# Kernel tuning notes

Hardware: AMD Instinct MI355X
Metric: run time of the kernel (lower is better)

Reference implementation:

```python
import jax, jax.numpy as jnp
import numpy as np

B, T, C = 4, 2048, 1024
H, Dh = 16, 64
EPS = 1e-5

def _layernorm(x, g, b):
    mu = jnp.mean(x, axis=-1, keepdims=True)
    var = jnp.mean(jnp.square(x - mu), axis=-1, keepdims=True)
    return (x - mu) * jax.lax.rsqrt(var + EPS) * g + b

def setup_inputs() -> dict:
    key = jax.random.key(0)
    ks = jax.random.split(key, 12)
    s = lambda fan_in: 1.0 / np.sqrt(fan_in)
    return {
        "x":  jax.random.normal(ks[0], (B, T, C), dtype=jnp.float32),
        "Wq": jax.random.uniform(ks[1], (C, H * Dh), jnp.float32, -s(C), s(C)),
        "Wk": jax.random.uniform(ks[2], (C, H * Dh), jnp.float32, -s(C), s(C)),
        "Wv": jax.random.uniform(ks[3], (C, H * Dh), jnp.float32, -s(C), s(C)),
        "Wo": jax.random.uniform(ks[4], (H * Dh, C), jnp.float32, -s(H * Dh), s(H * Dh)),
        "bo": jnp.zeros((C,), jnp.float32),
        "W1": jax.random.uniform(ks[5], (C, 4 * C), jnp.float32, -s(C), s(C)),
        "b1": jnp.zeros((4 * C,), jnp.float32),
        "W2": jax.random.uniform(ks[6], (4 * C, C), jnp.float32, -s(4 * C), s(4 * C)),
        "b2": jnp.zeros((C,), jnp.float32),
        "g1": jnp.ones((C,), jnp.float32),
        "be1": jnp.zeros((C,), jnp.float32),
        "g2": jnp.ones((C,), jnp.float32),
        "be2": jnp.zeros((C,), jnp.float32),
    }

def reference(x, Wq, Wk, Wv, Wo, bo, W1, b1, W2, b2, g1, be1, g2, be2):
    # --- pre-LN attention ---
    h = _layernorm(x, g1, be1)                                   # [B,T,C]
    q = (h @ Wq).reshape(B, T, H, Dh)                            # per-head projections fused
    k = (h @ Wk).reshape(B, T, H, Dh)
    v = (h @ Wv).reshape(B, T, H, Dh)
    scores = jnp.einsum('bqhd,bkhd->bhqk', q, k) * (Dh ** -0.5)  # [B,H,T,T]
    causal = jnp.tril(jnp.ones((T, T), dtype=bool))
    scores = jnp.where(causal, scores, -jnp.inf)
    wei = jax.nn.softmax(scores, axis=-1)                        # dropout p=0 (eval)
    attn = jnp.einsum('bhqk,bkhd->bqhd', wei, v).reshape(B, T, H * Dh)
    x = x + attn @ Wo + bo
    # --- pre-LN MLP ---
    h2 = _layernorm(x, g2, be2)
    x = x + jax.nn.relu(h2 @ W1 + b1) @ W2 + b2
    return x
```

## Files before the change

### kernel.cpp

```cpp
#include <hip/hip_runtime.h>
#include <hip/hip_bf16.h>

typedef __hip_bfloat16 bf16;
typedef __attribute__((ext_vector_type(8))) short short8;
typedef __attribute__((ext_vector_type(4))) float f32x4;

__device__ __forceinline__ float s2f(short s) {
    unsigned u = ((unsigned)(unsigned short)s) << 16;
    return __builtin_bit_cast(float, u);
}
__device__ __forceinline__ short f2s(float f) {
    bf16 h = __float2bfloat16(f);
    return __builtin_bit_cast(short, h);
}
__device__ __forceinline__ void gload_lds16(const void* g, void* l) {
    __builtin_amdgcn_global_load_lds(
        (const __attribute__((address_space(1))) unsigned int*)g,
        (__attribute__((address_space(3))) unsigned int*)l, 16, 0, 0);
}

__global__ __launch_bounds__(256) void tconv_kernel(const float* __restrict__ src,
                                                    short* __restrict__ dst,
                                                    int R, int C) {
    __shared__ short tile[64][65];
    const int r0 = blockIdx.y * 64, c0 = blockIdx.x * 64;
    const int t = threadIdx.x;
    const int lr = t >> 2, lc = (t & 3) * 16;
    const float* sp = src + (size_t)(r0 + lr) * C + c0 + lc;
#pragma unroll
    for (int q = 0; q < 4; q++) {
        f32x4 v = *(const f32x4*)(const void*)(sp + q * 4);
#pragma unroll
        for (int j = 0; j < 4; j++) tile[lr][lc + q * 4 + j] = f2s(v[j]);
    }
    __syncthreads();
    short8 o0, o1;
#pragma unroll
    for (int j = 0; j < 8; j++) { o0[j] = tile[lc + j][lr]; o1[j] = tile[lc + 8 + j][lr]; }
    short* dp = dst + (size_t)(c0 + lr) * R + r0 + lc;
    *(short8*)(void*)dp = o0;
    *(short8*)(void*)(dp + 8) = o1;
}

__global__ __launch_bounds__(256) void ln_kernel(const void* __restrict__ x, int x_f32,
                                                 const float* __restrict__ g,
                                                 const float* __restrict__ beta,
                                                 bf16* __restrict__ out) {
    const int row = blockIdx.x;
    const int t = threadIdx.x;
    float v[4];
    if (x_f32) {
        const float* xr = (const float*)x + (size_t)row * 1024 + t * 4;
        f32x4 xv = *(const f32x4*)(const void*)xr;
#pragma unroll
        for (int j = 0; j < 4; j++) v[j] = xv[j];
    } else {
        const short* xr = (const short*)x + (size_t)row * 1024 + t * 4;
#pragma unroll
        for (int j = 0; j < 4; j++) v[j] = s2f(xr[j]);
    }
    float s = 0.f, ss = 0.f;
#pragma unroll
    for (int j = 0; j < 4; j++) { s += v[j]; ss += v[j] * v[j]; }
#pragma unroll
    for (int off = 32; off >= 1; off >>= 1) {
        s += __shfl_xor(s, off);
        ss += __shfl_xor(ss, off);
    }
    __shared__ float red[8];
    const int wave = t >> 6;
    if ((t & 63) == 0) { red[wave] = s; red[4 + wave] = ss; }
    __syncthreads();
    s = red[0] + red[1] + red[2] + red[3];
    ss = red[4] + red[5] + red[6] + red[7];
    const float mu = s * (1.0f / 1024.0f);
    const float var = ss * (1.0f / 1024.0f) - mu * mu;
    const float rstd = rsqrtf(var + 1e-5f);
    bf16* orow = out + (size_t)row * 1024;
#pragma unroll
    for (int j = 0; j < 4; j++) {
        const int c = t * 4 + j;
        float hv = (v[j] - mu) * rstd * g[c] + beta[c];
        orow[c] = __float2bfloat16(hv);
    }
}

__global__ __launch_bounds__(256) void gemm128(const bf16* __restrict__ A,
                                               const bf16* __restrict__ Bt,
                                               const float* __restrict__ bias,
                                               const float* resid,
                                               void* Cp, int c_f32,
                                               int m_base, int N, int K,
                                               int relu_flag) {
    __shared__ short As[128 * 32];
    __shared__ short Bs[128 * 32];

    const int t = threadIdx.x;
    const int m0 = blockIdx.y * 128;
    const int n0 = blockIdx.x * 128;
    const int w = t >> 6;
    const int lane = t & 63;
    const int wm = (w >> 1) * 64;
    const int wn = (w & 1) * 64;

    const int ar = t >> 2, ak = (t & 3) * 8;
    const bf16* aA0 = A + (size_t)(m0 + ar) * K + ak;
    const bf16* aA1 = A + (size_t)(m0 + 64 + ar) * K + ak;
    const bf16* aB0 = Bt + (size_t)(n0 + ar) * K + ak;
    const bf16* aB1 = Bt + (size_t)(n0 + 64 + ar) * K + ak;
    short* ldsA0 = &As[w * 512];
    short* ldsA1 = &As[2048 + w * 512];
    short* ldsB0 = &Bs[w * 512];
    short* ldsB1 = &Bs[2048 + w * 512];

    const int l = lane & 15;
    const int lk = (lane >> 4) * 8;

    f32x4 acc[4][4] = {};

    for (int k0 = 0; k0 < K; k0 += 32) {
        __syncthreads();
        gload_lds16(aA0 + k0, ldsA0);
        gload_lds16(aA1 + k0, ldsA1);
        gload_lds16(aB0 + k0, ldsB0);
        gload_lds16(aB1 + k0, ldsB1);
        __syncthreads();

        short8 af[4], bfv[4];
#pragma unroll
        for (int mi = 0; mi < 4; mi++)
            af[mi] = *(const short8*)&As[(wm + mi * 16 + l) * 32 + lk];
#pragma unroll
        for (int ni = 0; ni < 4; ni++)
            bfv[ni] = *(const short8*)&Bs[(wn + ni * 16 + l) * 32 + lk];
#pragma unroll
        for (int mi = 0; mi < 4; mi++)
#pragma unroll
            for (int ni = 0; ni < 4; ni++)
                acc[mi][ni] = __builtin_amdgcn_mfma_f32_16x16x32_bf16(
                    af[mi], bfv[ni], acc[mi][ni], 0, 0, 0);
    }

    const int lrow4 = (lane >> 4) * 4;
#pragma unroll
    for (int mi = 0; mi < 4; mi++)
#pragma unroll
        for (int r = 0; r < 4; r++) {
            const int grow = m_base + m0 + wm + mi * 16 + lrow4 + r;
#pragma unroll
            for (int ni = 0; ni < 4; ni++) {
                const int gcol = n0 + wn + ni * 16 + l;
                float val = acc[mi][ni][r];
                if (bias) val += bias[gcol];
                if (relu_flag) val = fmaxf(val, 0.f);
                const size_t ci = (size_t)grow * N + gcol;
                if (resid) val += resid[ci];
                if (c_f32) ((float*)Cp)[ci] = val;
                else        ((short*)Cp)[ci] = f2s(val);
            }
        }
}

__global__ __launch_bounds__(256) void gemm64(const bf16* __restrict__ A,
                                              const bf16* __restrict__ Bt,
                                              const float* __restrict__ bias,
                                              const float* resid,
                                              void* Cp, int c_f32,
                                              int m_base, int N, int K,
                                              int relu_flag) {
    __shared__ short As[64 * 64];
    __shared__ short Bs[64 * 64];

    const int t = threadIdx.x;
    const int m0 = blockIdx.x * 64;
    const int n0 = blockIdx.y * 64;
    const int w = t >> 6;
    const int lane = t & 63;
    const int wm = (w >> 1) * 32;
    const int wn = (w & 1) * 32;

    const int sr = t >> 2, sk = (t & 3) * 8;
    const bf16* aA = A + (size_t)(m0 + sr) * K + sk;
    const bf16* aB = Bt + (size_t)(n0 + sr) * K + sk;
    short* ldsA0 = &As[w * 512];
    short* ldsA1 = &As[2048 + w * 512];
    short* ldsB0 = &Bs[w * 512];
    short* ldsB1 = &Bs[2048 + w * 512];

    const int l = lane & 15;
    const int lk = (lane >> 4) * 8;

    f32x4 acc[2][2] = {};

    for (int k0 = 0; k0 < K; k0 += 64) {
        __syncthreads();
        gload_lds16(aA + k0, ldsA0);
        gload_lds16(aA + k0 + 32, ldsA1);
        gload_lds16(aB + k0, ldsB0);
        gload_lds16(aB + k0 + 32, ldsB1);
        __syncthreads();
#pragma unroll
        for (int ks = 0; ks < 2; ks++) {
            short8 a0 = *(const short8*)&As[ks * 2048 + (wm + l) * 32 + lk];
            short8 a1 = *(const short8*)&As[ks * 2048 + (wm + 16 + l) * 32 + lk];
            short8 b0 = *(const short8*)&Bs[ks * 2048 + (wn + l) * 32 + lk];
            short8 b1 = *(const short8*)&Bs[ks * 2048 + (wn + 16 + l) * 32 + lk];
            acc[0][0] = __builtin_amdgcn_mfma_f32_16x16x32_bf16(a0, b0, acc[0][0], 0, 0, 0);
            acc[0][1] = __builtin_amdgcn_mfma_f32_16x16x32_bf16(a0, b1, acc[0][1], 0, 0, 0);
            acc[1][0] = __builtin_amdgcn_mfma_f32_16x16x32_bf16(a1, b0, acc[1][0], 0, 0, 0);
            acc[1][1] = __builtin_amdgcn_mfma_f32_16x16x32_bf16(a1, b1, acc[1][1], 0, 0, 0);
        }
    }

    const int lrow4 = (lane >> 4) * 4;
#pragma unroll
    for (int mi = 0; mi < 2; mi++)
#pragma unroll
        for (int r = 0; r < 4; r++) {
            const int grow = m_base + m0 + wm + mi * 16 + lrow4 + r;
#pragma unroll
            for (int ni = 0; ni < 2; ni++) {
                const int gcol = n0 + wn + ni * 16 + l;
                float val = acc[mi][ni][r];
                if (bias) val += bias[gcol];
                if (relu_flag) val = fmaxf(val, 0.f);
                const size_t ci = (size_t)grow * N + gcol;
                if (resid) val += resid[ci];
                if (c_f32) ((float*)Cp)[ci] = val;
                else        ((short*)Cp)[ci] = f2s(val);
            }
        }
}

__global__ __launch_bounds__(256) void attn_kernel(const bf16* __restrict__ qkv,
                                                   bf16* __restrict__ o) {
    __shared__ short Ks[64][72];
    __shared__ short Vt[64][72];
    __shared__ short Pl[4][32][72];

    const int bh = blockIdx.x;
    const int b = bh >> 4, h = bh & 15;
    const int qt = 15 - blockIdx.y;
    const int q0 = qt * 128;
    const size_t rbase = (size_t)b * 2048;
    const int hcol = h * 64;

    const int t = threadIdx.x;
    const int w = t >> 6;
    const int lane = t & 63;
    const int l = lane & 15;
    const int g = lane >> 4;
    const int sp = t >> 3;
    const int sb = (t & 7) * 8;

    const int qw0 = q0 + 32 * w;
    short8 qf[2][2];
#pragma unroll
    for (int mi = 0; mi < 2; mi++)
#pragma unroll
        for (int ks = 0; ks < 2; ks++) {
            const short* qp = (const short*)qkv +
                (rbase + qw0 + mi * 16 + l) * 3072 + hcol + ks * 32 + g * 8;
            short8 tv = *(const short8*)(const void*)qp;
            short8 sv;
#pragma unroll
            for (int e = 0; e < 8; e++) sv[e] = f2s(s2f(tv[e]) * 0.125f);
            qf[mi][ks] = sv;
        }

    f32x4 o_acc[2][4] = {};
    f32x4 l_acc[2] = {};
    short8 onesf;
    {
        const short ov = (l == 0) ? (short)0x3F80 : (short)0;
#pragma unroll
        for (int e = 0; e < 8; e++) onesf[e] = ov;
    }
    const f32x4 s_init = {-12.f, -12.f, -12.f, -12.f};

    const int kt_max = (q0 + 127) >> 6;
    for (int kt = 0; kt <= kt_max; kt++) {
        const int k0 = kt * 64;
        const short* kg = (const short*)qkv + (rbase + k0 + 2 * sp) * 3072 + 1024 + hcol + sb;
        const short* vg = (const short*)qkv + (rbase + k0 + 2 * sp) * 3072 + 2048 + hcol + sb;
        short8 kv0 = *(const short8*)(const void*)kg;
        short8 kv1 = *(const short8*)(const void*)(kg + 3072);
        short8 vv0 = *(const short8*)(const void*)vg;
        short8 vv1 = *(const short8*)(const void*)(vg + 3072);
        __syncthreads();
        *(short8*)&Ks[2 * sp][sb] = kv0;
        *(short8*)&Ks[2 * sp + 1][sb] = kv1;
        {
            const int key = 2 * sp;
            const int cbk = key >> 3;
            const int kin = key & 7;
#pragma unroll
            for (int j = 0; j < 8; j++) {
                const int d = sb + j;
                const int col = ((cbk ^ (d >> 3)) << 3) + kin;
                int pk = (int)(unsigned short)vv0[j] | ((int)(unsigned short)vv1[j] << 16);
                *(int*)(void*)&Vt[d][col] = pk;
            }
        }
        __syncthreads();

        if (k0 <= qw0 + 31) {
            const bool needMask = (k0 + 63 > qw0);
            f32x4 s_acc[2][4];
#pragma unroll
            for (int mi = 0; mi < 2; mi++)
#pragma unroll
                for (int ni = 0; ni < 4; ni++) s_acc[mi][ni] = s_init;
#pragma unroll
            for (int ks = 0; ks < 2; ks++) {
                short8 kf[4];
#pragma unroll
                for (int ni = 0; ni < 4; ni++)
                    kf[ni] = *(const short8*)&Ks[ni * 16 + l][ks * 32 + g * 8];
#pragma unroll
                for (int mi = 0; mi < 2; mi++)
#pragma unroll
                    for (int ni = 0; ni < 4; ni++)
                        s_acc[mi][ni] = __builtin_amdgcn_mfma_f32_16x16x32_bf16(
                            qf[mi][ks], kf[ni], s_acc[mi][ni], 0, 0, 0);
            }
#pragma unroll
            for (int mi = 0; mi < 2; mi++)
#pragma unroll
                for (int r = 0; r < 4; r++) {
                    const int qg = qw0 + mi * 16 + 4 * g + r;
#pragma unroll
                    for (int ni = 0; ni < 4; ni++) {
                        float s = s_acc[mi][ni][r];
                        if (needMask && (k0 + ni * 16 + l > qg)) s = -1e30f;
                        Pl[w][mi * 16 + 4 * g + r][ni * 16 + l] = f2s(__expf(s));
                    }
                }
#pragma unroll
            for (int ks = 0; ks < 2; ks++) {
                short8 pf[2], vf[4];
#pragma unroll
                for (int mi = 0; mi < 2; mi++)
                    pf[mi] = *(const short8*)&Pl[w][mi * 16 + l][ks * 32 + g * 8];
#pragma unroll
                for (int nd = 0; nd < 4; nd++) {
                    const int d = nd * 16 + l;
                    const int cb = ks * 4 + g;
                    vf[nd] = *(const short8*)&Vt[d][((cb ^ (d >> 3)) << 3)];
                }
#pragma unroll
                for (int mi = 0; mi < 2; mi++) {
                    l_acc[mi] = __builtin_amdgcn_mfma_f32_16x16x32_bf16(
                        pf[mi], onesf, l_acc[mi], 0, 0, 0);
#pragma unroll
                    for (int nd = 0; nd < 4; nd++)
                        o_acc[mi][nd] = __builtin_amdgcn_mfma_f32_16x16x32_bf16(
                            pf[mi], vf[nd], o_acc[mi][nd], 0, 0, 0);
                }
            }
        }
    }

#pragma unroll
    for (int mi = 0; mi < 2; mi++)
#pragma unroll
        for (int r = 0; r < 4; r++) {
            float lsum = __shfl(l_acc[mi][r], lane & 48);
            const float inv = 1.0f / lsum;
            const int qg = qw0 + mi * 16 + 4 * g + r;
            short* op = (short*)(void*)(o + (rbase + qg) * 1024 + hcol);
#pragma unroll
            for (int nd = 0; nd < 4; nd++)
                op[nd * 16 + l] = f2s(o_acc[mi][nd][r] * inv);
        }
}

extern "C" void kernel_launch(void* const* d_in, const int* in_sizes, int n_in,
                              void* d_out, int out_size, void* d_ws, size_t ws_size,
                              hipStream_t stream) {
    const float* x   = (const float*)d_in[0];
    const float* Wq  = (const float*)d_in[1];
    const float* Wk  = (const float*)d_in[2];
    const float* Wv  = (const float*)d_in[3];
    const float* Wo  = (const float*)d_in[4];
    const float* bo  = (const float*)d_in[5];
    const float* W1  = (const float*)d_in[6];
    const float* b1  = (const float*)d_in[7];
    const float* W2  = (const float*)d_in[8];
    const float* b2  = (const float*)d_in[9];
    const float* g1  = (const float*)d_in[10];
    const float* be1 = (const float*)d_in[11];
    const float* g2  = (const float*)d_in[12];
    const float* be2 = (const float*)d_in[13];

    char* ws = (char*)d_ws;
    const size_t MB = (size_t)1024 * 1024;
    bf16*  s0  = (bf16*)(ws);
    bf16*  qkv = (bf16*)(ws + 16 * MB);
    short* WoT = (short*)(ws + 16 * MB);
    short* W1T = (short*)(ws);
    short* W2T = (short*)(ws + 8 * MB);
    bf16*  h2  = (bf16*)(ws + 16 * MB);
    bf16*  m1  = (bf16*)(ws + 32 * MB);
    short* WT  = (short*)d_out;
    float* x1  = (float*)d_out;

    const int M = 8192, C = 1024, F = 4096, MH = 4096;

    tconv_kernel<<<dim3(16, 16), 256, 0, stream>>>(Wq, WT,                   C, C);
    tconv_kernel<<<dim3(16, 16), 256, 0, stream>>>(Wk, WT + 1024 * 1024,     C, C);
    tconv_kernel<<<dim3(16, 16), 256, 0, stream>>>(Wv, WT + 2 * 1024 * 1024, C, C);

    ln_kernel<<<M, 256, 0, stream>>>(x, 1, g1, be1, s0);

    gemm128<<<dim3(3072 / 128, M / 128), 256, 0, stream>>>(
        s0, (const bf16*)WT, nullptr, nullptr, qkv, 0, 0, 3072, C, 0);

    attn_kernel<<<dim3(64, 16), 256, 0, stream>>>(qkv, s0);

    tconv_kernel<<<dim3(16, 16), 256, 0, stream>>>(Wo, WoT, C, C);
    gemm64<<<dim3(M / 64, C / 64), 256, 0, stream>>>(
        s0, (const bf16*)WoT, bo, x, x1, 1, 0, C, C, 0);

    tconv_kernel<<<dim3(64, 16), 256, 0, stream>>>(W1, W1T, C, F);
    tconv_kernel<<<dim3(16, 64), 256, 0, stream>>>(W2, W2T, F, C);

    ln_kernel<<<M, 256, 0, stream>>>(x1, 1, g2, be2, h2);

    for (int half = 0; half < 2; half++) {
        const bf16* Ah = h2 + (size_t)half * MH * C;
        gemm128<<<dim3(F / 128, MH / 128), 256, 0, stream>>>(
            Ah, (const bf16*)W1T, b1, nullptr, m1, 0, 0, F, C, 1);
        gemm64<<<dim3(MH / 64, C / 64), 256, 0, stream>>>(
            m1, (const bf16*)W2T, b2, x1, d_out, 1, half * MH, C, F, 0);
    }
}
```

Baseline: 627.0 us.

## Use wave-per-row layernorm, async swizzled K loads, and gemm64 for all GEMMs

Layernorm now gives each wavefront one row with vectorized loads and stores, which drops the LDS reduction and block barrier. The attention kernel loads K tiles straight into LDS with global_load_lds using an XOR-swizzled layout instead of staging them through registers. gemm128 is removed, so the QKV and W1 GEMMs now use the 64x64 tiled gemm64. Smaller tiles cut reuse per block but launch more blocks, which may help occupancy or may raise memory traffic.

```diff
diff --git a/kernel.cpp b/kernel.cpp
--- a/kernel.cpp
+++ b/kernel.cpp
@@ -3,6 +3,7 @@
 
 typedef __hip_bfloat16 bf16;
 typedef __attribute__((ext_vector_type(8))) short short8;
+typedef __attribute__((ext_vector_type(4))) short s16x4;
 typedef __attribute__((ext_vector_type(4))) float f32x4;
 
 __device__ __forceinline__ float s2f(short s) {
@@ -42,123 +43,46 @@
     *(short8*)(void*)(dp + 8) = o1;
 }
 
-__global__ __launch_bounds__(256) void ln_kernel(const void* __restrict__ x, int x_f32,
+__global__ __launch_bounds__(256) void ln_kernel(const float* __restrict__ x,
                                                  const float* __restrict__ g,
                                                  const float* __restrict__ beta,
                                                  bf16* __restrict__ out) {
-    const int row = blockIdx.x;
     const int t = threadIdx.x;
-    float v[4];
-    if (x_f32) {
-        const float* xr = (const float*)x + (size_t)row * 1024 + t * 4;
-        f32x4 xv = *(const f32x4*)(const void*)xr;
-#pragma unroll
-        for (int j = 0; j < 4; j++) v[j] = xv[j];
-    } else {
-        const short* xr = (const short*)x + (size_t)row * 1024 + t * 4;
-#pragma unroll
-        for (int j = 0; j < 4; j++) v[j] = s2f(xr[j]);
-    }
+    const int w = t >> 6, lane = t & 63;
+    const int row = blockIdx.x * 4 + w;
+    const float* xr = x + (size_t)row * 1024;
+    float v[16];
     float s = 0.f, ss = 0.f;
 #pragma unroll
-    for (int j = 0; j < 4; j++) { s += v[j]; ss += v[j] * v[j]; }
+    for (int p = 0; p < 4; p++) {
+        f32x4 xv = *(const f32x4*)(const void*)(xr + p * 256 + lane * 4);
+#pragma unroll
+        for (int j = 0; j < 4; j++) {
+            v[p * 4 + j] = xv[j];
+            s += xv[j];
+            ss += xv[j] * xv[j];
+        }
+    }
 #pragma unroll
     for (int off = 32; off >= 1; off >>= 1) {
         s += __shfl_xor(s, off);
         ss += __shfl_xor(ss, off);
     }
-    __shared__ float red[8];
-    const int wave = t >> 6;
-    if ((t & 63) == 0) { red[wave] = s; red[4 + wave] = ss; }
-    __syncthreads();
-    s = red[0] + red[1] + red[2] + red[3];
-    ss = red[4] + red[5] + red[6] + red[7];
     const float mu = s * (1.0f / 1024.0f);
     const float var = ss * (1.0f / 1024.0f) - mu * mu;
     const float rstd = rsqrtf(var + 1e-5f);
-    bf16* orow = out + (size_t)row * 1024;
-#pragma unroll
-    for (int j = 0; j < 4; j++) {
-        const int c = t * 4 + j;
-        float hv = (v[j] - mu) * rstd * g[c] + beta[c];
-        orow[c] = __float2bfloat16(hv);
-    }
-}
-
-__global__ __launch_bounds__(256) void gemm128(const bf16* __restrict__ A,
-                                               const bf16* __restrict__ Bt,
-                                               const float* __restrict__ bias,
-                                               const float* resid,
-                                               void* Cp, int c_f32,
-                                               int m_base, int N, int K,
-                                               int relu_flag) {
-    __shared__ short As[128 * 32];
-    __shared__ short Bs[128 * 32];
-
-    const int t = threadIdx.x;
-    const int m0 = blockIdx.y * 128;
-    const int n0 = blockIdx.x * 128;
-    const int w = t >> 6;
-    const int lane = t & 63;
-    const int wm = (w >> 1) * 64;
-    const int wn = (w & 1) * 64;
-
-    const int ar = t >> 2, ak = (t & 3) * 8;
-    const bf16* aA0 = A + (size_t)(m0 + ar) * K + ak;
-    const bf16* aA1 = A + (size_t)(m0 + 64 + ar) * K + ak;
-    const bf16* aB0 = Bt + (size_t)(n0 + ar) * K + ak;
-    const bf16* aB1 = Bt + (size_t)(n0 + 64 + ar) * K + ak;
-    short* ldsA0 = &As[w * 512];
-    short* ldsA1 = &As[2048 + w * 512];
-    short* ldsB0 = &Bs[w * 512];
-    short* ldsB1 = &Bs[2048 + w * 512];
-
-    const int l = lane & 15;
-    const int lk = (lane >> 4) * 8;
-
-    f32x4 acc[4][4] = {};
-
-    for (int k0 = 0; k0 < K; k0 += 32) {
-        __syncthreads();
-        gload_lds16(aA0 + k0, ldsA0);
-        gload_lds16(aA1 + k0, ldsA1);
-        gload_lds16(aB0 + k0, ldsB0);
-        gload_lds16(aB1 + k0, ldsB1);
-        __syncthreads();
-
-        short8 af[4], bfv[4];
-#pragma unroll
-        for (int mi = 0; mi < 4; mi++)
-            af[mi] = *(const short8*)&As[(wm + mi * 16 + l) * 32 + lk];
-#pragma unroll
-        for (int ni = 0; ni < 4; ni++)
-            bfv[ni] = *(const short8*)&Bs[(wn + ni * 16 + l) * 32 + lk];
-#pragma unroll
-        for (int mi = 0; mi < 4; mi++)
-#pragma unroll
-            for (int ni = 0; ni < 4; ni++)
-                acc[mi][ni] = __builtin_amdgcn_mfma_f32_16x16x32_bf16(
-                    af[mi], bfv[ni], acc[mi][ni], 0, 0, 0);
-    }
-
-    const int lrow4 = (lane >> 4) * 4;
-#pragma unroll
-    for (int mi = 0; mi < 4; mi++)
-#pragma unroll
-        for (int r = 0; r < 4; r++) {
-            const int grow = m_base + m0 + wm + mi * 16 + lrow4 + r;
-#pragma unroll
-            for (int ni = 0; ni < 4; ni++) {
-                const int gcol = n0 + wn + ni * 16 + l;
-                float val = acc[mi][ni][r];
-                if (bias) val += bias[gcol];
-                if (relu_flag) val = fmaxf(val, 0.f);
-                const size_t ci = (size_t)grow * N + gcol;
-                if (resid) val += resid[ci];
-                if (c_f32) ((float*)Cp)[ci] = val;
-                else        ((short*)Cp)[ci] = f2s(val);
-            }
-        }
+    short* orow = (short*)(void*)(out + (size_t)row * 1024);
+#pragma unroll
+    for (int p = 0; p < 4; p++) {
+        const int c = p * 256 + lane * 4;
+        f32x4 gv = *(const f32x4*)(const void*)(g + c);
+        f32x4 bv = *(const f32x4*)(const void*)(beta + c);
+        s16x4 o;
+#pragma unroll
+        for (int j = 0; j < 4; j++)
+            o[j] = f2s((v[p * 4 + j] - mu) * rstd * gv[j] + bv[j]);
+        *(s16x4*)(void*)(orow + c) = o;
+    }
 }
 
 __global__ __launch_bounds__(256) void gemm64(const bf16* __restrict__ A,
@@ -234,7 +158,7 @@
 
 __global__ __launch_bounds__(256) void attn_kernel(const bf16* __restrict__ qkv,
                                                    bf16* __restrict__ o) {
-    __shared__ short Ks[64][72];
+    __shared__ short KsF[64 * 64];
     __shared__ short Vt[64][72];
     __shared__ short Pl[4][32][72];
 
@@ -268,6 +192,13 @@
             qf[mi][ks] = sv;
         }
 
+    const int key_a = w * 16 + (lane >> 3);
+    const int kd = (lane & 7) ^ ((lane >> 3) & 7);
+    const short* kgA = (const short*)qkv + (rbase + key_a) * 3072 + 1024 + hcol + kd * 8;
+    const short* kgB = kgA + 8 * 3072;
+    short* kdstA = &KsF[w * 1024];
+    short* kdstB = &KsF[w * 1024 + 512];
+
     f32x4 o_acc[2][4] = {};
     f32x4 l_acc[2] = {};
     short8 onesf;
@@ -281,15 +212,12 @@
     const int kt_max = (q0 + 127) >> 6;
     for (int kt = 0; kt <= kt_max; kt++) {
         const int k0 = kt * 64;
-        const short* kg = (const short*)qkv + (rbase + k0 + 2 * sp) * 3072 + 1024 + hcol + sb;
         const short* vg = (const short*)qkv + (rbase + k0 + 2 * sp) * 3072 + 2048 + hcol + sb;
-        short8 kv0 = *(const short8*)(const void*)kg;
-        short8 kv1 = *(const short8*)(const void*)(kg + 3072);
         short8 vv0 = *(const short8*)(const void*)vg;
         short8 vv1 = *(const short8*)(const void*)(vg + 3072);
         __syncthreads();
-        *(short8*)&Ks[2 * sp][sb] = kv0;
-        *(short8*)&Ks[2 * sp + 1][sb] = kv1;
+        gload_lds16(kgA + (size_t)k0 * 3072, kdstA);
+        gload_lds16(kgB + (size_t)k0 * 3072, kdstB);
         {
             const int key = 2 * sp;
             const int cbk = key >> 3;
@@ -315,8 +243,11 @@
             for (int ks = 0; ks < 2; ks++) {
                 short8 kf[4];
 #pragma unroll
-                for (int ni = 0; ni < 4; ni++)
-                    kf[ni] = *(const short8*)&Ks[ni * 16 + l][ks * 32 + g * 8];
+                for (int ni = 0; ni < 4; ni++) {
+                    const int key = ni * 16 + l;
+                    const int c = key * 8 + ((ks * 4 + g) ^ (key & 7));
+                    kf[ni] = *(const short8*)&KsF[c * 8];
+                }
 #pragma unroll
                 for (int mi = 0; mi < 2; mi++)
 #pragma unroll
@@ -411,9 +342,9 @@
     tconv_kernel<<<dim3(16, 16), 256, 0, stream>>>(Wk, WT + 1024 * 1024,     C, C);
     tconv_kernel<<<dim3(16, 16), 256, 0, stream>>>(Wv, WT + 2 * 1024 * 1024, C, C);
 
-    ln_kernel<<<M, 256, 0, stream>>>(x, 1, g1, be1, s0);
-
-    gemm128<<<dim3(3072 / 128, M / 128), 256, 0, stream>>>(
+    ln_kernel<<<M / 4, 256, 0, stream>>>(x, g1, be1, s0);
+
+    gemm64<<<dim3(M / 64, 3072 / 64), 256, 0, stream>>>(
         s0, (const bf16*)WT, nullptr, nullptr, qkv, 0, 0, 3072, C, 0);
 
     attn_kernel<<<dim3(64, 16), 256, 0, stream>>>(qkv, s0);
@@ -425,11 +356,11 @@
     tconv_kernel<<<dim3(64, 16), 256, 0, stream>>>(W1, W1T, C, F);
     tconv_kernel<<<dim3(16, 64), 256, 0, stream>>>(W2, W2T, F, C);
 
-    ln_kernel<<<M, 256, 0, stream>>>(x1, 1, g2, be2, h2);
+    ln_kernel<<<M / 4, 256, 0, stream>>>(x1, g2, be2, h2);
 
     for (int half = 0; half < 2; half++) {
         const bf16* Ah = h2 + (size_t)half * MH * C;
-        gemm128<<<dim3(F / 128, MH / 128), 256, 0, stream>>>(
+        gemm64<<<dim3(MH / 64, F / 64), 256, 0, stream>>>(
             Ah, (const bf16*)W1T, b1, nullptr, m1, 0, 0, F, C, 1);
         gemm64<<<dim3(MH / 64, C / 64), 256, 0, stream>>>(
             m1, (const bf16*)W2T, b2, x1, d_out, 1, half * MH, C, F, 0);
```

Result: faster. 589.1 us (-6.0%).
